# Optimization experiments

Hardware: AMD Instinct MI355X
Metric: run time of the kernel (lower is better)

Reference implementation:

```python
import jax, jax.numpy as jnp
from jax import lax
import numpy as np

ARG_NAMES = ('x w1 b1 bn1_g bn1_b bn1_m bn1_v w2 b2 bn2_g bn2_b bn2_m bn2_v w3 b3 w4 b4 '
             'attn_w attn_b attn_u g0_w1 g0_b1 g0_w2 g0_b2 g1_w1 g1_b1 g1_w2 g1_b2 '
             'g2_w1 g2_b1 g2_w2 g2_b2 c_w1 c_b1 c_w2 c_b2 c_w3 c_b3 c_w4 c_b4').split()


def _conv1d(x, w, b, stride, pad):
    # x: [N, C, L], w: [O, I, K]
    y = lax.conv_general_dilated(x, w, (stride,), [(pad, pad)],
                                 dimension_numbers=('NCH', 'OIH', 'NCH'))
    return y + b[None, :, None]


def _bn(x, g, b, m, v, eps=1e-5):
    # eval-mode BatchNorm1d over channel dim of [N, C, L]
    inv = g / jnp.sqrt(v + eps)
    return (x - m[None, :, None]) * inv[None, :, None] + b[None, :, None]


def _forward(x, w1, b1, bn1_g, bn1_b, bn1_m, bn1_v, w2, b2, bn2_g, bn2_b, bn2_m, bn2_v,
             w3, b3, w4, b4, attn_w, attn_b, attn_u,
             g0_w1, g0_b1, g0_w2, g0_b2, g1_w1, g1_b1, g1_w2, g1_b2,
             g2_w1, g2_b1, g2_w2, g2_b2,
             c_w1, c_b1, c_w2, c_b2, c_w3, c_b3, c_w4, c_b4):
    B, S, C, T = x.shape  # [batch, crops, channels=64, time=400]
    h = x.reshape(-1, C, T)
    # CNN stack (dropout = identity in eval)
    h = _bn(jax.nn.elu(_conv1d(h, w1, b1, 2, 1)), bn1_g, bn1_b, bn1_m, bn1_v)   # [N,64,192]
    h = _bn(jax.nn.elu(_conv1d(h, w2, b2, 2, 0)), bn2_g, bn2_b, bn2_m, bn2_v)   # [N,64,87]
    h = jax.nn.elu(_conv1d(h, w3, b3, 1, 0))                                    # [N,64,82]
    h = lax.reduce_window(h, 0.0, lax.add, (1, 1, 3), (1, 1, 2), 'VALID') / 3.0  # [N,64,40]
    h = jax.nn.elu(_conv1d(h, w4, b4, 1, 0))                                    # [N,64,35]
    h = h.reshape(B, S, C, -1)  # [B, S, 64, 35]
    # Attention pooling over the crop dim (dim=1), sum=True
    v = jnp.tanh(jnp.einsum('bsch,hd->bscd', h, attn_w) + attn_b)
    alphas = jax.nn.softmax(jnp.einsum('bscd,d->bsc', v, attn_u), axis=1)
    h = jax.nn.elu((h * alphas[..., None]).sum(axis=1))  # [B, 64, 35]
    # GIN over complete 64-node graph (self-loops included, eps=0):
    # aggregation per node == sum over all nodes of the graph
    def gin(h, W1, B1, W2, B2):
        agg = h + h.sum(axis=1, keepdims=True)
        return jax.nn.relu(agg @ W1 + B1) @ W2 + B2
    h = jax.nn.relu(gin(h, g0_w1, g0_b1, g0_w2, g0_b2))
    h = jax.nn.relu(gin(h, g1_w1, g1_b1, g1_w2, g1_b2))
    h = gin(h, g2_w1, g2_b1, g2_w2, g2_b2)  # no act after last layer
    # Classifier
    f = h.reshape(B, -1)  # [B, 2240]
    f = jax.nn.elu(f @ c_w1 + c_b1)
    f = jax.nn.elu(f @ c_w2 + c_b2)
    f = jax.nn.elu(f @ c_w3 + c_b3)
    return f @ c_w4 + c_b4  # [B, 2]


def setup_inputs() -> dict:
    key = jax.random.key(0)
    ks = iter(jax.random.split(key, 64))
    def rn(shape, s=0.05):
        return jax.random.normal(next(ks), shape, dtype=jnp.float32) * s
    d = {}
    d['x'] = jax.random.normal(next(ks), (32, 16, 64, 400), dtype=jnp.float32)
    d['w1'] = rn((64, 64, 20)); d['b1'] = rn((64,))
    d['bn1_g'] = jnp.ones((64,), jnp.float32); d['bn1_b'] = jnp.zeros((64,), jnp.float32)
    d['bn1_m'] = jnp.zeros((64,), jnp.float32); d['bn1_v'] = jnp.ones((64,), jnp.float32)
    d['w2'] = rn((64, 64, 20)); d['b2'] = rn((64,))
    d['bn2_g'] = jnp.ones((64,), jnp.float32); d['bn2_b'] = jnp.zeros((64,), jnp.float32)
    d['bn2_m'] = jnp.zeros((64,), jnp.float32); d['bn2_v'] = jnp.ones((64,), jnp.float32)
    d['w3'] = rn((64, 64, 6)); d['b3'] = rn((64,))
    d['w4'] = rn((64, 64, 6)); d['b4'] = rn((64,))
    d['attn_w'] = rn((35, 256), 0.1); d['attn_b'] = rn((256,), 0.1); d['attn_u'] = rn((256,), 0.1)
    d['g0_w1'] = rn((35, 256)); d['g0_b1'] = rn((256,))
    d['g0_w2'] = rn((256, 256)); d['g0_b2'] = rn((256,))
    d['g1_w1'] = rn((256, 256)); d['g1_b1'] = rn((256,))
    d['g1_w2'] = rn((256, 256)); d['g1_b2'] = rn((256,))
    d['g2_w1'] = rn((256, 35)); d['g2_b1'] = rn((35,))
    d['g2_w2'] = rn((35, 35)); d['g2_b2'] = rn((35,))
    d['c_w1'] = rn((2240, 256)); d['c_b1'] = rn((256,))
    d['c_w2'] = rn((256, 64)); d['c_b2'] = rn((64,))
    d['c_w3'] = rn((64, 16)); d['c_b3'] = rn((16,))
    d['c_w4'] = rn((16, 2)); d['c_b4'] = rn((2,))
    return d


def reference(x, w1, b1, bn1_g, bn1_b, bn1_m, bn1_v, w2, b2, bn2_g, bn2_b, bn2_m, bn2_v,
              w3, b3, w4, b4, attn_w, attn_b, attn_u,
              g0_w1, g0_b1, g0_w2, g0_b2, g1_w1, g1_b1, g1_w2, g1_b2,
              g2_w1, g2_b1, g2_w2, g2_b2,
              c_w1, c_b1, c_w2, c_b2, c_w3, c_b3, c_w4, c_b4):
    return _forward(x, w1, b1, bn1_g, bn1_b, bn1_m, bn1_v, w2, b2, bn2_g, bn2_b, bn2_m, bn2_v,
                    w3, b3, w4, b4, attn_w, attn_b, attn_u,
                    g0_w1, g0_b1, g0_w2, g0_b2, g1_w1, g1_b1, g1_w2, g1_b2,
                    g2_w1, g2_b1, g2_w2, g2_b2,
                    c_w1, c_b1, c_w2, c_b2, c_w3, c_b3, c_w4, c_b4)
```

## Files before the change

kernel.cpp:

```cpp
#include <hip/hip_runtime.h>
#include <math.h>

typedef __attribute__((ext_vector_type(8))) __bf16 bf16x8;
typedef __attribute__((ext_vector_type(4))) __bf16 bf16x4;
typedef __attribute__((ext_vector_type(4))) float f32x4;

__device__ __forceinline__ float elu_f(float v) {
    return v > 0.f ? v : (expf(v) - 1.f);
}

__global__ __launch_bounds__(256) void prep_weights(
    const float* __restrict__ w1, const float* __restrict__ w2,
    const float* __restrict__ w3, const float* __restrict__ w4,
    __bf16* __restrict__ t1, __bf16* __restrict__ t2,
    __bf16* __restrict__ t3, __bf16* __restrict__ t4)
{
    int idx = blockIdx.x * 256 + threadIdx.x;
    if (idx < 81920) {
        int k = idx / 4096, r = idx - k * 4096, co = r >> 6, ci = r & 63;
        t1[idx] = (__bf16)w1[(co * 64 + ci) * 20 + k];
    } else if (idx < 163840) {
        int j = idx - 81920;
        int k = j / 4096, r = j - k * 4096, co = r >> 6, ci = r & 63;
        t2[j] = (__bf16)w2[(co * 64 + ci) * 20 + k];
    } else if (idx < 188416) {
        int j = idx - 163840;
        int k = j / 4096, r = j - k * 4096, co = r >> 6, ci = r & 63;
        t3[j] = (__bf16)w3[(co * 64 + ci) * 6 + k];
    } else if (idx < 212992) {
        int j = idx - 188416;
        int k = j / 4096, r = j - k * 4096, co = r >> 6, ci = r & 63;
        t4[j] = (__bf16)w4[(co * 64 + ci) * 6 + k];
    }
}

__global__ __launch_bounds__(256) void prep_tr(
    const float* __restrict__ g0w1, const float* __restrict__ g0w2,
    const float* __restrict__ g1w1, const float* __restrict__ g1w2,
    const float* __restrict__ g2w1, const float* __restrict__ g2w2,
    __bf16* __restrict__ d0, __bf16* __restrict__ d1, __bf16* __restrict__ d2,
    __bf16* __restrict__ d3, __bf16* __restrict__ d4, __bf16* __restrict__ d5)
{
    int bid = blockIdx.x;
    const float* src; __bf16* dst; int K, O, Kpad, Opad, tile;
    if (bid < 4)       { src = g0w1; dst = d0; K = 35;   O = 256; Kpad = 64;   Opad = 256; tile = bid; }
    else if (bid < 20) { src = g0w2; dst = d1; K = 256;  O = 256; Kpad = 256;  Opad = 256; tile = bid - 4; }
    else if (bid < 36) { src = g1w1; dst = d2; K = 256;  O = 256; Kpad = 256;  Opad = 256; tile = bid - 20; }
    else if (bid < 52) { src = g1w2; dst = d3; K = 256;  O = 256; Kpad = 256;  Opad = 256; tile = bid - 36; }
    else if (bid < 56) { src = g2w1; dst = d4; K = 256;  O = 35;  Kpad = 256;  Opad = 64;  tile = bid - 52; }
    else               { src = g2w2; dst = d5; K = 35;   O = 35;  Kpad = 64;   Opad = 64;  tile = 0; }
    int ktiles = Kpad >> 6;
    int ot = tile / ktiles, kt = tile - ot * ktiles;
    int k0 = kt * 64, o0 = ot * 64;
    size_t LOFF = (size_t)Opad * Kpad;
    __shared__ float tl[64][68];
    int c = threadIdx.x & 63, rr = threadIdx.x >> 6;
    #pragma unroll
    for (int it = 0; it < 16; ++it) {
        int r = rr + it * 4;
        int kk = k0 + r, oo = o0 + c;
        tl[r][c] = (kk < K && oo < O) ? src[(size_t)kk * O + oo] : 0.f;
    }
    __syncthreads();
    #pragma unroll
    for (int it = 0; it < 16; ++it) {
        int r = rr + it * 4;
        float v = tl[c][r];
        __bf16 hi = (__bf16)v;
        float lo = v - (float)hi;
        size_t pos = (size_t)(o0 + r) * Kpad + k0 + c;
        dst[pos] = hi;
        dst[LOFF + pos] = (__bf16)lo;
    }
}

__global__ __launch_bounds__(512, 2) void conv1_mfma(
    const float* __restrict__ x, const __bf16* __restrict__ wT,
    const float* __restrict__ bias,
    const float* __restrict__ bn_g, const float* __restrict__ bn_b,
    const float* __restrict__ bn_m, const float* __restrict__ bn_v,
    __bf16* __restrict__ y)
{
    constexpr int LIN = 400, LOUT = 192, PAD = 1;
    constexpr int ROWS = 201;
    __shared__ __align__(16) __bf16 sx[2 * ROWS * 72];
    __shared__ __align__(16) __bf16 sw[2 * 64 * 72];

    const int tid = threadIdx.x;
    const int n = blockIdx.x;
    const int wave = tid >> 6, lane = tid & 63;
    const int m = lane & 15, quad = lane >> 4;
    const int tile = wave >> 1;
    const int coh  = (wave & 1) * 32;

    {
        const float* xg = x + (size_t)n * 64 * LIN;
        if (tid < 128) {
            int v = (tid >> 6) ? 401 : 0;
            sx[((v & 1) * ROWS + (v >> 1)) * 72 + (tid & 63)] = (__bf16)0.f;
        }
        constexpr int ITEMS = 16 * (LIN / 4);
        #pragma unroll
        for (int it = 0; it < 4; ++it) {
            int idx = it * 512 + tid;
            if (idx < ITEMS) {
                int jj = idx & 3;
                int g  = (idx >> 2) & 15;
                int q  = (idx >> 6) * 4 + jj;
                const float* xp = xg + (size_t)(4 * g) * LIN + 4 * q;
                float fa[4][4];
                #pragma unroll
                for (int u = 0; u < 4; ++u)
                    *(float4*)&fa[u][0] = *(const float4*)(xp + (size_t)u * LIN);
                #pragma unroll
                for (int e = 0; e < 4; ++e) {
                    int v = 4 * q + e + PAD;
                    bf16x4 wv = { (__bf16)fa[0][e], (__bf16)fa[1][e],
                                  (__bf16)fa[2][e], (__bf16)fa[3][e] };
                    *(bf16x4*)&sx[((v & 1) * ROWS + (v >> 1)) * 72 + 4 * g] = wv;
                }
            }
        }
    }

    f32x4 acc[3][2];
    #pragma unroll
    for (int mi = 0; mi < 3; ++mi)
        #pragma unroll
        for (int nj = 0; nj < 2; ++nj)
            acc[mi][nj] = (f32x4){0.f, 0.f, 0.f, 0.f};

    for (int kb = 0; kb < 20; kb += 2) {
        if (kb) __syncthreads();
        #pragma unroll
        for (int i = 0; i < 2; ++i) {
            int idx = i * 512 + tid;
            int r = idx >> 3, p = idx & 7;
            *(uint4*)(sw + (size_t)r * 72 + p * 8) =
                *(const uint4*)(wT + (size_t)(kb + (r >> 6)) * 4096 + (r & 63) * 64 + p * 8);
        }
        __syncthreads();

        #pragma unroll
        for (int kp2 = 0; kp2 < 2; ++kp2) {
            const int kp = kb + kp2;
            const int buf = kp & 1, rowoff = kp >> 1;
            const __bf16* abase = sx + ((size_t)buf * ROWS + tile * 48 + m + rowoff) * 72;
            const __bf16* bbase = sw + (size_t)(kp2 * 64 + coh + m) * 72;
            #pragma unroll
            for (int s = 0; s < 2; ++s) {
                bf16x8 af[3], bfr[2];
                #pragma unroll
                for (int mi = 0; mi < 3; ++mi)
                    af[mi] = *(const bf16x8*)(abase + mi * (16 * 72) + s * 32 + quad * 8);
                #pragma unroll
                for (int nj = 0; nj < 2; ++nj)
                    bfr[nj] = *(const bf16x8*)(bbase + nj * (16 * 72) + s * 32 + quad * 8);
                #pragma unroll
                for (int mi = 0; mi < 3; ++mi)
                    #pragma unroll
                    for (int nj = 0; nj < 2; ++nj)
                        acc[mi][nj] = __builtin_amdgcn_mfma_f32_16x16x32_bf16(
                            af[mi], bfr[nj], acc[mi][nj], 0, 0, 0);
            }
        }
    }

    #pragma unroll
    for (int nj = 0; nj < 2; ++nj) {
        const int co = coh + nj * 16 + m;
        const float bi = bias[co];
        const float inv   = bn_g[co] / sqrtf(bn_v[co] + 1e-5f);
        const float shift = bn_b[co] - bn_m[co] * inv;
        #pragma unroll
        for (int mi = 0; mi < 3; ++mi)
            #pragma unroll
            for (int r = 0; r < 4; ++r) {
                int t = tile * 48 + mi * 16 + quad * 4 + r;
                float v = elu_f(acc[mi][nj][r] + bi) * inv + shift;
                y[((size_t)n * LOUT + t) * 64 + co] = (__bf16)v;
            }
    }
}

__global__ __launch_bounds__(512, 2) void conv234_fused(
    const __bf16* __restrict__ h1,
    const __bf16* __restrict__ wT2, const float* __restrict__ b2,
    const float* __restrict__ bn2g, const float* __restrict__ bn2b,
    const float* __restrict__ bn2m, const float* __restrict__ bn2v,
    const __bf16* __restrict__ wT3, const float* __restrict__ b3,
    const __bf16* __restrict__ wT4, const float* __restrict__ b4,
    __bf16* __restrict__ h4)
{
    __shared__ __align__(16) __bf16 bufA[2 * 96 * 72];
    __shared__ __align__(16) __bf16 bufB[87 * 72];

    const int tid = threadIdx.x;
    const int n = blockIdx.x;
    const int wave = tid >> 6, lane = tid & 63;
    const int m = lane & 15, quad = lane >> 4;
    const int th  = wave >> 2;
    const int coq = wave & 3;

    {
        const __bf16* src = h1 + (size_t)n * 192 * 64;
        #pragma unroll
        for (int it = 0; it < 3; ++it) {
            int idx = it * 512 + tid;
            int v = idx >> 3, c8 = (idx & 7) * 8;
            *(uint4*)(bufA + ((size_t)(v & 1) * 96 + (v >> 1)) * 72 + c8) =
                *(const uint4*)(src + (size_t)v * 64 + c8);
        }
    }
    __syncthreads();

    {
        const __bf16* wb = wT2 + (size_t)(coq * 16 + m) * 64 + quad * 8;
        bf16x8 bw[20][2];
        #pragma unroll
        for (int kp = 0; kp < 20; ++kp)
            #pragma unroll
            for (int s = 0; s < 2; ++s)
                bw[kp][s] = *(const bf16x8*)(wb + (size_t)kp * 4096 + s * 32);

        f32x4 acc[3];
        #pragma unroll
        for (int mi = 0; mi < 3; ++mi) acc[mi] = (f32x4){0.f, 0.f, 0.f, 0.f};

        #pragma unroll
        for (int kp = 0; kp < 20; ++kp) {
            const int buf = kp & 1, rowoff = kp >> 1;
            const int r0 = th * 48 + m + rowoff;
            #pragma unroll
            for (int s = 0; s < 2; ++s) {
                bf16x8 af[3];
                #pragma unroll
                for (int mi = 0; mi < 3; ++mi) {
                    int rr = r0 + mi * 16; if (rr > 95) rr = 95;
                    af[mi] = *(const bf16x8*)(bufA + ((size_t)buf * 96 + rr) * 72 + s * 32 + quad * 8);
                }
                #pragma unroll
                for (int mi = 0; mi < 3; ++mi)
                    acc[mi] = __builtin_amdgcn_mfma_f32_16x16x32_bf16(
                        af[mi], bw[kp][s], acc[mi], 0, 0, 0);
            }
        }

        const int co = coq * 16 + m;
        const float bi = b2[co];
        float inv = bn2g[co] / sqrtf(bn2v[co] + 1e-5f);
        float shift = bn2b[co] - bn2m[co] * inv;
        #pragma unroll
        for (int mi = 0; mi < 3; ++mi)
            #pragma unroll
            for (int r = 0; r < 4; ++r) {
                int t = th * 48 + mi * 16 + quad * 4 + r;
                if (t < 87) {
                    float v = elu_f(acc[mi][r] + bi) * inv + shift;
                    bufB[t * 72 + co] = (__bf16)v;
                }
            }
    }
    __syncthreads();

    {
        const __bf16* wb = wT3 + (size_t)(coq * 16 + m) * 64 + quad * 8;
        bf16x8 bw[6][2];
        #pragma unroll
        for (int kp = 0; kp < 6; ++kp)
            #pragma unroll
            for (int s = 0; s < 2; ++s)
                bw[kp][s] = *(const bf16x8*)(wb + (size_t)kp * 4096 + s * 32);

        f32x4 acc[3];
        #pragma unroll
        for (int mi = 0; mi < 3; ++mi) acc[mi] = (f32x4){0.f, 0.f, 0.f, 0.f};

        #pragma unroll
        for (int kp = 0; kp < 6; ++kp) {
            const int r0 = th * 48 + m + kp;
            #pragma unroll
            for (int s = 0; s < 2; ++s) {
                bf16x8 af[3];
                #pragma unroll
                for (int mi = 0; mi < 3; ++mi) {
                    int rr = r0 + mi * 16; if (rr > 86) rr = 86;
                    af[mi] = *(const bf16x8*)(bufB + (size_t)rr * 72 + s * 32 + quad * 8);
                }
                #pragma unroll
                for (int mi = 0; mi < 3; ++mi)
                    acc[mi] = __builtin_amdgcn_mfma_f32_16x16x32_bf16(
                        af[mi], bw[kp][s], acc[mi], 0, 0, 0);
            }
        }

        const int co = coq * 16 + m;
        const float bi = b3[co];
        #pragma unroll
        for (int mi = 0; mi < 3; ++mi)
            #pragma unroll
            for (int r = 0; r < 4; ++r) {
                int t = th * 48 + mi * 16 + quad * 4 + r;
                if (t < 82)
                    bufA[t * 72 + co] = (__bf16)elu_f(acc[mi][r] + bi);
            }
    }
    __syncthreads();

    #pragma unroll
    for (int it = 0; it < 5; ++it) {
        int idx = it * 512 + tid;
        int t = idx >> 6, co = idx & 63;
        float v = ((float)bufA[(2 * t) * 72 + co] + (float)bufA[(2 * t + 1) * 72 + co] +
                   (float)bufA[(2 * t + 2) * 72 + co]) * (1.f / 3.f);
        bufB[t * 72 + co] = (__bf16)v;
    }
    __syncthreads();

    if (wave < 4) {
        const int co0 = wave * 16;
        const __bf16* wb = wT4 + (size_t)(co0 + m) * 64 + quad * 8;
        bf16x8 bw[6][2];
        #pragma unroll
        for (int kp = 0; kp < 6; ++kp)
            #pragma unroll
            for (int s = 0; s < 2; ++s)
                bw[kp][s] = *(const bf16x8*)(wb + (size_t)kp * 4096 + s * 32);

        f32x4 acc4[3];
        #pragma unroll
        for (int mi = 0; mi < 3; ++mi) acc4[mi] = (f32x4){0.f, 0.f, 0.f, 0.f};

        #pragma unroll
        for (int kp = 0; kp < 6; ++kp) {
            const int r0 = m + kp;
            #pragma unroll
            for (int s = 0; s < 2; ++s) {
                bf16x8 af[3];
                #pragma unroll
                for (int mi = 0; mi < 3; ++mi) {
                    int rr = r0 + mi * 16; if (rr > 39) rr = 39;
                    af[mi] = *(const bf16x8*)(bufB + (size_t)rr * 72 + s * 32 + quad * 8);
                }
                #pragma unroll
                for (int mi = 0; mi < 3; ++mi)
                    acc4[mi] = __builtin_amdgcn_mfma_f32_16x16x32_bf16(
                        af[mi], bw[kp][s], acc4[mi], 0, 0, 0);
            }
        }

        const int co = co0 + m;
        const float bi = b4[co];
        #pragma unroll
        for (int mi = 0; mi < 3; ++mi)
            #pragma unroll
            for (int r = 0; r < 4; ++r) {
                int t = mi * 16 + quad * 4 + r;
                if (t < 35)
                    h4[((size_t)n * 35 + t) * 64 + co] = (__bf16)elu_f(acc4[mi][r] + bi);
            }
    }
}

__global__ __launch_bounds__(256) void attn_pool_k(
    const __bf16* __restrict__ h, const float* __restrict__ W,
    const float* __restrict__ ab, const float* __restrict__ u,
    float* __restrict__ out)
{
    __shared__ float sW[35 * 256];
    __shared__ float sh[4][16 * 35 + 5];
    const int tid = threadIdx.x;
    const int pair0 = blockIdx.x * 4;
    for (int i = tid; i < 35 * 256; i += 256) sW[i] = W[i];
    for (int i = tid; i < 4 * 560; i += 256) {
        int q = i / 560, r = i - q * 560;
        int s = r / 35, t = r - s * 35;
        int bc = pair0 + q, b = bc >> 6, c = bc & 63;
        sh[q][s * 35 + t] = (float)h[(((size_t)b * 16 + s) * 35 + t) * 64 + c];
    }
    __syncthreads();

    const int wave = tid >> 6, lane = tid & 63;
    const int bc = pair0 + wave;
    const float* shw = sh[wave];

    float myu[4], myb[4];
    #pragma unroll
    for (int p = 0; p < 4; ++p) { myu[p] = u[lane + 64 * p]; myb[p] = ab[lane + 64 * p]; }

    float dot[16][4];
    #pragma unroll
    for (int s = 0; s < 16; ++s)
        #pragma unroll
        for (int p = 0; p < 4; ++p) dot[s][p] = myb[p];

    for (int t = 0; t < 35; ++t) {
        float w0 = sW[t * 256 + lane];
        float w1 = sW[t * 256 + lane + 64];
        float w2 = sW[t * 256 + lane + 128];
        float w3 = sW[t * 256 + lane + 192];
        #pragma unroll
        for (int s = 0; s < 16; ++s) {
            float hv = shw[s * 35 + t];
            dot[s][0] = fmaf(hv, w0, dot[s][0]);
            dot[s][1] = fmaf(hv, w1, dot[s][1]);
            dot[s][2] = fmaf(hv, w2, dot[s][2]);
            dot[s][3] = fmaf(hv, w3, dot[s][3]);
        }
    }

    float sc[16];
    #pragma unroll
    for (int s = 0; s < 16; ++s) {
        float v = tanhf(dot[s][0]) * myu[0] + tanhf(dot[s][1]) * myu[1]
                + tanhf(dot[s][2]) * myu[2] + tanhf(dot[s][3]) * myu[3];
        #pragma unroll
        for (int off = 1; off < 64; off <<= 1) v += __shfl_xor(v, off, 64);
        sc[s] = v;
    }

    float mx = sc[0];
    #pragma unroll
    for (int s = 1; s < 16; ++s) mx = fmaxf(mx, sc[s]);
    float e[16], sum = 0.f;
    #pragma unroll
    for (int s = 0; s < 16; ++s) { e[s] = expf(sc[s] - mx); sum += e[s]; }
    float inv = 1.f / sum;

    if (lane < 35) {
        float acc = 0.f;
        #pragma unroll
        for (int s = 0; s < 16; ++s) acc = fmaf(shw[s * 35 + lane], e[s] * inv, acc);
        out[(size_t)bc * 35 + lane] = elu_f(acc);
    }
}

#define APLANE (64 * 264)

__device__ __forceinline__ void gin_gemm_dev(
    const __bf16* As,
    const __bf16* __restrict__ Wg, int Kpad, int wlo, int Kout,
    const float* __restrict__ bias,
    int mode, __bf16* Ad, float* __restrict__ outg)
{
    const int lane = threadIdx.x & 63;
    const int wave = threadIdx.x >> 6;
    const int o0 = wave * 32;
    if (o0 >= ((Kout + 63) & ~63)) return;
    const int m = lane & 15, quad = lane >> 4;

    f32x4 acc[4][2];
    #pragma unroll
    for (int mi = 0; mi < 4; ++mi)
        #pragma unroll
        for (int nj = 0; nj < 2; ++nj)
            acc[mi][nj] = (f32x4){0.f, 0.f, 0.f, 0.f};

    for (int k0 = 0; k0 < Kpad; k0 += 32) {
        bf16x8 ah[4], al[4], bh[2], bl[2];
        #pragma unroll
        for (int mi = 0; mi < 4; ++mi) {
            const __bf16* ap = As + (size_t)(mi * 16 + m) * 264 + k0 + quad * 8;
            ah[mi] = *(const bf16x8*)ap;
            al[mi] = *(const bf16x8*)(ap + APLANE);
        }
        #pragma unroll
        for (int nj = 0; nj < 2; ++nj) {
            const __bf16* wp = Wg + (size_t)(o0 + nj * 16 + m) * Kpad + k0 + quad * 8;
            bh[nj] = *(const bf16x8*)wp;
            bl[nj] = *(const bf16x8*)(wp + wlo);
        }
        #pragma unroll
        for (int mi = 0; mi < 4; ++mi)
            #pragma unroll
            for (int nj = 0; nj < 2; ++nj) {
                acc[mi][nj] = __builtin_amdgcn_mfma_f32_16x16x32_bf16(
                    al[mi], bh[nj], acc[mi][nj], 0, 0, 0);
                acc[mi][nj] = __builtin_amdgcn_mfma_f32_16x16x32_bf16(
                    ah[mi], bl[nj], acc[mi][nj], 0, 0, 0);
                acc[mi][nj] = __builtin_amdgcn_mfma_f32_16x16x32_bf16(
                    ah[mi], bh[nj], acc[mi][nj], 0, 0, 0);
            }
    }

    #pragma unroll
    for (int nj = 0; nj < 2; ++nj) {
        const int o = o0 + nj * 16 + m;
        const bool ovalid = (o < Kout);
        const float bi = ovalid ? bias[o] : 0.f;
        float v[4][4];
        #pragma unroll
        for (int mi = 0; mi < 4; ++mi)
            #pragma unroll
            for (int r = 0; r < 4; ++r)
                v[mi][r] = acc[mi][nj][r] + bi;
        if (mode == 2) {
            if (ovalid) {
                #pragma unroll
                for (int mi = 0; mi < 4; ++mi)
                    #pragma unroll
                    for (int r = 0; r < 4; ++r)
                        outg[(size_t)(mi * 16 + quad * 4 + r) * Kout + o] = v[mi][r];
            }
        } else {
            float s = 0.f;
            #pragma unroll
            for (int mi = 0; mi < 4; ++mi)
                #pragma unroll
                for (int r = 0; r < 4; ++r) {
                    float rv = ovalid ? fmaxf(v[mi][r], 0.f) : 0.f;
                    v[mi][r] = rv;
                    s += rv;
                }
            if (mode == 1) {
                s += __shfl_xor(s, 16, 64);
                s += __shfl_xor(s, 32, 64);
            } else {
                s = 0.f;
            }
            #pragma unroll
            for (int mi = 0; mi < 4; ++mi)
                #pragma unroll
                for (int r = 0; r < 4; ++r) {
                    float a = v[mi][r] + s;
                    __bf16 hi = (__bf16)a;
                    size_t pos = (size_t)(mi * 16 + quad * 4 + r) * 264 + o;
                    Ad[pos] = hi;
                    Ad[APLANE + pos] = (__bf16)(a - (float)hi);
                }
        }
    }
}

__global__ __launch_bounds__(512) void gin_fused(
    const float* __restrict__ ha,
    const __bf16* __restrict__ gW0a, const __bf16* __restrict__ gW0b,
    const __bf16* __restrict__ gW1a, const __bf16* __restrict__ gW1b,
    const __bf16* __restrict__ gW2a, const __bf16* __restrict__ gW2b,
    const float* __restrict__ b0a, const float* __restrict__ b0b,
    const float* __restrict__ b1a, const float* __restrict__ b1b,
    const float* __restrict__ b2a, const float* __restrict__ b2b,
    float* __restrict__ H3)
{
    const int b = blockIdx.x, tid = threadIdx.x;
    __shared__ __align__(16) __bf16 sA[2][2 * APLANE];
    __shared__ float sS[64];
    const float* hab = ha + (size_t)b * 2240;

    if (tid < 64) {
        float s = 0.f;
        if (tid < 35)
            for (int n = 0; n < 64; ++n) s += hab[n * 35 + tid];
        sS[tid] = s;
    }
    __syncthreads();
    for (int idx = tid; idx < 64 * 64; idx += 512) {
        int n = idx >> 6, k = idx & 63;
        float a = (k < 35) ? hab[n * 35 + k] + sS[k] : 0.f;
        __bf16 hi = (__bf16)a;
        sA[0][n * 264 + k] = hi;
        sA[0][APLANE + n * 264 + k] = (__bf16)(a - (float)hi);
    }
    __syncthreads();

    gin_gemm_dev(sA[0], gW0a, 64,  16384, 256, b0a, 0, sA[1], nullptr); __syncthreads();
    gin_gemm_dev(sA[1], gW0b, 256, 65536, 256, b0b, 1, sA[0], nullptr); __syncthreads();
    gin_gemm_dev(sA[0], gW1a, 256, 65536, 256, b1a, 0, sA[1], nullptr); __syncthreads();
    gin_gemm_dev(sA[1], gW1b, 256, 65536, 256, b1b, 1, sA[0], nullptr); __syncthreads();
    gin_gemm_dev(sA[0], gW2a, 256, 16384, 35,  b2a, 0, sA[1], nullptr); __syncthreads();
    gin_gemm_dev(sA[1], gW2b, 64,  4096,  35,  b2b, 2, nullptr, H3 + (size_t)b * 2240);
}

__global__ __launch_bounds__(256) void cls1_part_k(
    const float* __restrict__ H3, const float* __restrict__ w1,
    float* __restrict__ s1p)
{
    const int b  = blockIdx.x;
    const int kc = blockIdx.y;
    const int k0 = kc * 140;
    __shared__ float sH[140];
    const int tid = threadIdx.x;
    if (tid < 140) sH[tid] = H3[(size_t)b * 2240 + k0 + tid];
    __syncthreads();
    const int o = (tid >> 6) * 64 + (tid & 63);
    float a0 = 0.f, a1 = 0.f, a2 = 0.f, a3 = 0.f;
    const float* wr = w1 + (size_t)k0 * 256 + o;
    #pragma unroll
    for (int k = 0; k < 140; k += 4) {
        a0 = fmaf(sH[k],     wr[(size_t)k * 256],       a0);
        a1 = fmaf(sH[k + 1], wr[(size_t)(k + 1) * 256], a1);
        a2 = fmaf(sH[k + 2], wr[(size_t)(k + 2) * 256], a2);
        a3 = fmaf(sH[k + 3], wr[(size_t)(k + 3) * 256], a3);
    }
    s1p[((size_t)kc * 32 + b) * 256 + o] = a0 + a1 + a2 + a3;
}

__global__ __launch_bounds__(256) void cls234_k(
    const float* __restrict__ s1p, const float* __restrict__ b1,
    const float* __restrict__ w2, const float* __restrict__ b2,
    const float* __restrict__ w3, const float* __restrict__ b3,
    const float* __restrict__ w4, const float* __restrict__ b4,
    float* __restrict__ out)
{
    const int b = blockIdx.x, tid = threadIdx.x;
    __shared__ float s1[256];
    __shared__ float part[4][64];
    __shared__ float s2[64];
    __shared__ float s3[16];
    {
        float acc = b1[tid];
        #pragma unroll
        for (int kc = 0; kc < 16; ++kc)
            acc += s1p[((size_t)kc * 32 + b) * 256 + tid];
        s1[tid] = elu_f(acc);
    }
    __syncthreads();
    {
        int kg = tid >> 6, o = tid & 63;
        float acc = 0.f;
        for (int k = kg * 64; k < kg * 64 + 64; ++k)
            acc = fmaf(s1[k], w2[k * 64 + o], acc);
        part[kg][o] = acc;
    }
    __syncthreads();
    if (tid < 64) {
        float acc = part[0][tid] + part[1][tid] + part[2][tid] + part[3][tid] + b2[tid];
        s2[tid] = elu_f(acc);
    }
    __syncthreads();
    if (tid < 16) {
        float acc = b3[tid];
        for (int k = 0; k < 64; ++k) acc = fmaf(s2[k], w3[k * 16 + tid], acc);
        s3[tid] = elu_f(acc);
    }
    __syncthreads();
    if (tid < 2) {
        float acc = b4[tid];
        for (int k = 0; k < 16; ++k) acc = fmaf(s3[k], w4[k * 2 + tid], acc);
        out[b * 2 + tid] = acc;
    }
}

extern "C" void kernel_launch(void* const* d_in, const int* in_sizes, int n_in,
                              void* d_out, int out_size, void* d_ws, size_t ws_size,
                              hipStream_t stream)
{
    const float* x     = (const float*)d_in[0];
    const float* w1    = (const float*)d_in[1];
    const float* b1    = (const float*)d_in[2];
    const float* bn1_g = (const float*)d_in[3];
    const float* bn1_b = (const float*)d_in[4];
    const float* bn1_m = (const float*)d_in[5];
    const float* bn1_v = (const float*)d_in[6];
    const float* w2    = (const float*)d_in[7];
    const float* b2    = (const float*)d_in[8];
    const float* bn2_g = (const float*)d_in[9];
    const float* bn2_b = (const float*)d_in[10];
    const float* bn2_m = (const float*)d_in[11];
    const float* bn2_v = (const float*)d_in[12];
    const float* w3    = (const float*)d_in[13];
    const float* b3    = (const float*)d_in[14];
    const float* w4    = (const float*)d_in[15];
    const float* b4    = (const float*)d_in[16];
    const float* attn_w = (const float*)d_in[17];
    const float* attn_b = (const float*)d_in[18];
    const float* attn_u = (const float*)d_in[19];
    const float* g0_w1 = (const float*)d_in[20];
    const float* g0_b1 = (const float*)d_in[21];
    const float* g0_w2 = (const float*)d_in[22];
    const float* g0_b2 = (const float*)d_in[23];
    const float* g1_w1 = (const float*)d_in[24];
    const float* g1_b1 = (const float*)d_in[25];
    const float* g1_w2 = (const float*)d_in[26];
    const float* g1_b2 = (const float*)d_in[27];
    const float* g2_w1 = (const float*)d_in[28];
    const float* g2_b1 = (const float*)d_in[29];
    const float* g2_w2 = (const float*)d_in[30];
    const float* g2_b2 = (const float*)d_in[31];
    const float* c_w1  = (const float*)d_in[32];
    const float* c_b1  = (const float*)d_in[33];
    const float* c_w2  = (const float*)d_in[34];
    const float* c_b2  = (const float*)d_in[35];
    const float* c_w3  = (const float*)d_in[36];
    const float* c_b3  = (const float*)d_in[37];
    const float* c_w4  = (const float*)d_in[38];
    const float* c_b4  = (const float*)d_in[39];
    float* out = (float*)d_out;

    char* ws = (char*)d_ws;
    __bf16* wT1  = (__bf16*)(ws + 0);
    __bf16* wT2  = (__bf16*)(ws + 163840);
    __bf16* wT3  = (__bf16*)(ws + 327680);
    __bf16* wT4  = (__bf16*)(ws + 376832);
    __bf16* h1   = (__bf16*)(ws + 425984);
    __bf16* h4   = (__bf16*)(ws + 13008896);
    float*  ha   = (float*)(ws + 15302656);
    __bf16* gW0a = (__bf16*)(ws + 15589376);
    __bf16* gW0b = (__bf16*)(ws + 15654912);
    __bf16* gW1a = (__bf16*)(ws + 15917056);
    __bf16* gW1b = (__bf16*)(ws + 16179200);
    __bf16* gW2a = (__bf16*)(ws + 16441344);
    __bf16* gW2b = (__bf16*)(ws + 16506880);
    float*  H3   = (float*)(ws + 16523264);
    float*  s1p  = (float*)(ws + 16809984);

    prep_weights<<<dim3(832), dim3(256), 0, stream>>>(w1, w2, w3, w4, wT1, wT2, wT3, wT4);
    prep_tr<<<dim3(57), dim3(256), 0, stream>>>(g0_w1, g0_w2, g1_w1, g1_w2, g2_w1, g2_w2,
                                                gW0a, gW0b, gW1a, gW1b, gW2a, gW2b);

    conv1_mfma<<<dim3(512), dim3(512), 0, stream>>>(
        x, wT1, b1, bn1_g, bn1_b, bn1_m, bn1_v, h1);

    conv234_fused<<<dim3(512), dim3(512), 0, stream>>>(
        h1, wT2, b2, bn2_g, bn2_b, bn2_m, bn2_v, wT3, b3, wT4, b4, h4);

    attn_pool_k<<<dim3(512), dim3(256), 0, stream>>>(h4, attn_w, attn_b, attn_u, ha);

    gin_fused<<<dim3(32), dim3(512), 0, stream>>>(
        ha, gW0a, gW0b, gW1a, gW1b, gW2a, gW2b,
        g0_b1, g0_b2, g1_b1, g1_b2, g2_b1, g2_b2, H3);

    cls1_part_k<<<dim3(32, 16), dim3(256), 0, stream>>>(H3, c_w1, s1p);
    cls234_k<<<dim3(32), dim3(256), 0, stream>>>(s1p, c_b1, c_w2, c_b2, c_w3, c_b3,
                                                 c_w4, c_b4, out);
}
```

Baseline: 298.6 us.

## Fuse conv1 into conv2-4 kernel and merge weight-prep launches

Merges the conv1 kernel into the fused conv2-4 kernel so conv1's output stays in shared memory (aliased over the input staging buffer) instead of round-tripping h1 through global memory. Conv2 weights are now staged through shared memory in k-pairs rather than held in 40 register fragments. The two weight-prep kernels are combined into one launch. The trade-offs are extra barriers in the conv2 loop, higher shared-memory use per block, and a more register-heavy single kernel that may limit occupancy.

```diff
diff --git a/kernel.cpp b/kernel.cpp
--- a/kernel.cpp
+++ b/kernel.cpp
@@ -9,39 +9,40 @@
     return v > 0.f ? v : (expf(v) - 1.f);
 }
 
-__global__ __launch_bounds__(256) void prep_weights(
+__global__ __launch_bounds__(256) void prep_all(
     const float* __restrict__ w1, const float* __restrict__ w2,
     const float* __restrict__ w3, const float* __restrict__ w4,
     __bf16* __restrict__ t1, __bf16* __restrict__ t2,
-    __bf16* __restrict__ t3, __bf16* __restrict__ t4)
-{
-    int idx = blockIdx.x * 256 + threadIdx.x;
-    if (idx < 81920) {
-        int k = idx / 4096, r = idx - k * 4096, co = r >> 6, ci = r & 63;
-        t1[idx] = (__bf16)w1[(co * 64 + ci) * 20 + k];
-    } else if (idx < 163840) {
-        int j = idx - 81920;
-        int k = j / 4096, r = j - k * 4096, co = r >> 6, ci = r & 63;
-        t2[j] = (__bf16)w2[(co * 64 + ci) * 20 + k];
-    } else if (idx < 188416) {
-        int j = idx - 163840;
-        int k = j / 4096, r = j - k * 4096, co = r >> 6, ci = r & 63;
-        t3[j] = (__bf16)w3[(co * 64 + ci) * 6 + k];
-    } else if (idx < 212992) {
-        int j = idx - 188416;
-        int k = j / 4096, r = j - k * 4096, co = r >> 6, ci = r & 63;
-        t4[j] = (__bf16)w4[(co * 64 + ci) * 6 + k];
-    }
-}
-
-__global__ __launch_bounds__(256) void prep_tr(
+    __bf16* __restrict__ t3, __bf16* __restrict__ t4,
     const float* __restrict__ g0w1, const float* __restrict__ g0w2,
     const float* __restrict__ g1w1, const float* __restrict__ g1w2,
     const float* __restrict__ g2w1, const float* __restrict__ g2w2,
     __bf16* __restrict__ d0, __bf16* __restrict__ d1, __bf16* __restrict__ d2,
     __bf16* __restrict__ d3, __bf16* __restrict__ d4, __bf16* __restrict__ d5)
 {
-    int bid = blockIdx.x;
+    __shared__ float tl[64][68];
+    const int bigbid = blockIdx.x;
+    if (bigbid < 832) {
+        int idx = bigbid * 256 + threadIdx.x;
+        if (idx < 81920) {
+            int k = idx / 4096, r = idx - k * 4096, co = r >> 6, ci = r & 63;
+            t1[idx] = (__bf16)w1[(co * 64 + ci) * 20 + k];
+        } else if (idx < 163840) {
+            int j = idx - 81920;
+            int k = j / 4096, r = j - k * 4096, co = r >> 6, ci = r & 63;
+            t2[j] = (__bf16)w2[(co * 64 + ci) * 20 + k];
+        } else if (idx < 188416) {
+            int j = idx - 163840;
+            int k = j / 4096, r = j - k * 4096, co = r >> 6, ci = r & 63;
+            t3[j] = (__bf16)w3[(co * 64 + ci) * 6 + k];
+        } else if (idx < 212992) {
+            int j = idx - 188416;
+            int k = j / 4096, r = j - k * 4096, co = r >> 6, ci = r & 63;
+            t4[j] = (__bf16)w4[(co * 64 + ci) * 6 + k];
+        }
+        return;
+    }
+    int bid = bigbid - 832;
     const float* src; __bf16* dst; int K, O, Kpad, Opad, tile;
     if (bid < 4)       { src = g0w1; dst = d0; K = 35;   O = 256; Kpad = 64;   Opad = 256; tile = bid; }
     else if (bid < 20) { src = g0w2; dst = d1; K = 256;  O = 256; Kpad = 256;  Opad = 256; tile = bid - 4; }
@@ -53,7 +54,6 @@
     int ot = tile / ktiles, kt = tile - ot * ktiles;
     int k0 = kt * 64, o0 = ot * 64;
     size_t LOFF = (size_t)Opad * Kpad;
-    __shared__ float tl[64][68];
     int c = threadIdx.x & 63, rr = threadIdx.x >> 6;
     #pragma unroll
     for (int it = 0; it < 16; ++it) {
@@ -74,24 +74,31 @@
     }
 }
 
-__global__ __launch_bounds__(512, 2) void conv1_mfma(
-    const float* __restrict__ x, const __bf16* __restrict__ wT,
-    const float* __restrict__ bias,
-    const float* __restrict__ bn_g, const float* __restrict__ bn_b,
-    const float* __restrict__ bn_m, const float* __restrict__ bn_v,
-    __bf16* __restrict__ y)
+__global__ __launch_bounds__(512, 2) void conv1234_fused(
+    const float* __restrict__ x, const __bf16* __restrict__ wT1,
+    const float* __restrict__ b1,
+    const float* __restrict__ bn1g, const float* __restrict__ bn1b,
+    const float* __restrict__ bn1m, const float* __restrict__ bn1v,
+    const __bf16* __restrict__ wT2, const float* __restrict__ b2,
+    const float* __restrict__ bn2g, const float* __restrict__ bn2b,
+    const float* __restrict__ bn2m, const float* __restrict__ bn2v,
+    const __bf16* __restrict__ wT3, const float* __restrict__ b3,
+    const __bf16* __restrict__ wT4, const float* __restrict__ b4,
+    __bf16* __restrict__ h4)
 {
-    constexpr int LIN = 400, LOUT = 192, PAD = 1;
+    constexpr int LIN = 400, PAD = 1;
     constexpr int ROWS = 201;
-    __shared__ __align__(16) __bf16 sx[2 * ROWS * 72];
+    __shared__ __align__(16) __bf16 smem[2 * ROWS * 72];
     __shared__ __align__(16) __bf16 sw[2 * 64 * 72];
+
+    __bf16* sx   = smem;
+    __bf16* bufA = smem;
+    __bf16* bufB = smem + 2 * 96 * 72;
 
     const int tid = threadIdx.x;
     const int n = blockIdx.x;
     const int wave = tid >> 6, lane = tid & 63;
     const int m = lane & 15, quad = lane >> 4;
-    const int tile = wave >> 1;
-    const int coh  = (wave & 1) * 32;
 
     {
         const float* xg = x + (size_t)n * 64 * LIN;
@@ -123,126 +130,109 @@
         }
     }
 
-    f32x4 acc[3][2];
-    #pragma unroll
-    for (int mi = 0; mi < 3; ++mi)
-        #pragma unroll
-        for (int nj = 0; nj < 2; ++nj)
-            acc[mi][nj] = (f32x4){0.f, 0.f, 0.f, 0.f};
-
-    for (int kb = 0; kb < 20; kb += 2) {
-        if (kb) __syncthreads();
-        #pragma unroll
-        for (int i = 0; i < 2; ++i) {
-            int idx = i * 512 + tid;
-            int r = idx >> 3, p = idx & 7;
-            *(uint4*)(sw + (size_t)r * 72 + p * 8) =
-                *(const uint4*)(wT + (size_t)(kb + (r >> 6)) * 4096 + (r & 63) * 64 + p * 8);
-        }
-        __syncthreads();
-
-        #pragma unroll
-        for (int kp2 = 0; kp2 < 2; ++kp2) {
-            const int kp = kb + kp2;
-            const int buf = kp & 1, rowoff = kp >> 1;
-            const __bf16* abase = sx + ((size_t)buf * ROWS + tile * 48 + m + rowoff) * 72;
-            const __bf16* bbase = sw + (size_t)(kp2 * 64 + coh + m) * 72;
-            #pragma unroll
-            for (int s = 0; s < 2; ++s) {
-                bf16x8 af[3], bfr[2];
-                #pragma unroll
-                for (int mi = 0; mi < 3; ++mi)
-                    af[mi] = *(const bf16x8*)(abase + mi * (16 * 72) + s * 32 + quad * 8);
-                #pragma unroll
-                for (int nj = 0; nj < 2; ++nj)
-                    bfr[nj] = *(const bf16x8*)(bbase + nj * (16 * 72) + s * 32 + quad * 8);
-                #pragma unroll
-                for (int mi = 0; mi < 3; ++mi)
+    const int tile = wave >> 1;
+    const int coh  = (wave & 1) * 32;
+    {
+        f32x4 acc[3][2];
+        #pragma unroll
+        for (int mi = 0; mi < 3; ++mi)
+            #pragma unroll
+            for (int nj = 0; nj < 2; ++nj)
+                acc[mi][nj] = (f32x4){0.f, 0.f, 0.f, 0.f};
+
+        for (int kb = 0; kb < 20; kb += 2) {
+            if (kb) __syncthreads();
+            #pragma unroll
+            for (int i = 0; i < 2; ++i) {
+                int idx = i * 512 + tid;
+                int r = idx >> 3, p = idx & 7;
+                *(uint4*)(sw + (size_t)r * 72 + p * 8) =
+                    *(const uint4*)(wT1 + (size_t)(kb + (r >> 6)) * 4096 + (r & 63) * 64 + p * 8);
+            }
+            __syncthreads();
+
+            #pragma unroll
+            for (int kp2 = 0; kp2 < 2; ++kp2) {
+                const int kp = kb + kp2;
+                const int buf = kp & 1, rowoff = kp >> 1;
+                const __bf16* abase = sx + ((size_t)buf * ROWS + tile * 48 + m + rowoff) * 72;
+                const __bf16* bbase = sw + (size_t)(kp2 * 64 + coh + m) * 72;
+                #pragma unroll
+                for (int s = 0; s < 2; ++s) {
+                    bf16x8 af[3], bfr[2];
+                    #pragma unroll
+                    for (int mi = 0; mi < 3; ++mi)
+                        af[mi] = *(const bf16x8*)(abase + mi * (16 * 72) + s * 32 + quad * 8);
                     #pragma unroll
                     for (int nj = 0; nj < 2; ++nj)
-                        acc[mi][nj] = __builtin_amdgcn_mfma_f32_16x16x32_bf16(
-                            af[mi], bfr[nj], acc[mi][nj], 0, 0, 0);
-            }
-        }
-    }
-
-    #pragma unroll
-    for (int nj = 0; nj < 2; ++nj) {
-        const int co = coh + nj * 16 + m;
-        const float bi = bias[co];
-        const float inv   = bn_g[co] / sqrtf(bn_v[co] + 1e-5f);
-        const float shift = bn_b[co] - bn_m[co] * inv;
-        #pragma unroll
-        for (int mi = 0; mi < 3; ++mi)
-            #pragma unroll
-            for (int r = 0; r < 4; ++r) {
-                int t = tile * 48 + mi * 16 + quad * 4 + r;
-                float v = elu_f(acc[mi][nj][r] + bi) * inv + shift;
-                y[((size_t)n * LOUT + t) * 64 + co] = (__bf16)v;
-            }
-    }
-}
-
-__global__ __launch_bounds__(512, 2) void conv234_fused(
-    const __bf16* __restrict__ h1,
-    const __bf16* __restrict__ wT2, const float* __restrict__ b2,
-    const float* __restrict__ bn2g, const float* __restrict__ bn2b,
-    const float* __restrict__ bn2m, const float* __restrict__ bn2v,
-    const __bf16* __restrict__ wT3, const float* __restrict__ b3,
-    const __bf16* __restrict__ wT4, const float* __restrict__ b4,
-    __bf16* __restrict__ h4)
-{
-    __shared__ __align__(16) __bf16 bufA[2 * 96 * 72];
-    __shared__ __align__(16) __bf16 bufB[87 * 72];
-
-    const int tid = threadIdx.x;
-    const int n = blockIdx.x;
-    const int wave = tid >> 6, lane = tid & 63;
-    const int m = lane & 15, quad = lane >> 4;
+                        bfr[nj] = *(const bf16x8*)(bbase + nj * (16 * 72) + s * 32 + quad * 8);
+                    #pragma unroll
+                    for (int mi = 0; mi < 3; ++mi)
+                        #pragma unroll
+                        for (int nj = 0; nj < 2; ++nj)
+                            acc[mi][nj] = __builtin_amdgcn_mfma_f32_16x16x32_bf16(
+                                af[mi], bfr[nj], acc[mi][nj], 0, 0, 0);
+                }
+            }
+        }
+        __syncthreads();
+
+        #pragma unroll
+        for (int nj = 0; nj < 2; ++nj) {
+            const int co = coh + nj * 16 + m;
+            const float bi = b1[co];
+            const float inv   = bn1g[co] / sqrtf(bn1v[co] + 1e-5f);
+            const float shift = bn1b[co] - bn1m[co] * inv;
+            #pragma unroll
+            for (int mi = 0; mi < 3; ++mi)
+                #pragma unroll
+                for (int r = 0; r < 4; ++r) {
+                    int t = tile * 48 + mi * 16 + quad * 4 + r;
+                    float v = elu_f(acc[mi][nj][r] + bi) * inv + shift;
+                    bufA[((size_t)(t & 1) * 96 + (t >> 1)) * 72 + co] = (__bf16)v;
+                }
+        }
+    }
+    __syncthreads();
+
     const int th  = wave >> 2;
     const int coq = wave & 3;
-
     {
-        const __bf16* src = h1 + (size_t)n * 192 * 64;
-        #pragma unroll
-        for (int it = 0; it < 3; ++it) {
-            int idx = it * 512 + tid;
-            int v = idx >> 3, c8 = (idx & 7) * 8;
-            *(uint4*)(bufA + ((size_t)(v & 1) * 96 + (v >> 1)) * 72 + c8) =
-                *(const uint4*)(src + (size_t)v * 64 + c8);
-        }
-    }
-    __syncthreads();
-
-    {
-        const __bf16* wb = wT2 + (size_t)(coq * 16 + m) * 64 + quad * 8;
-        bf16x8 bw[20][2];
-        #pragma unroll
-        for (int kp = 0; kp < 20; ++kp)
-            #pragma unroll
-            for (int s = 0; s < 2; ++s)
-                bw[kp][s] = *(const bf16x8*)(wb + (size_t)kp * 4096 + s * 32);
-
         f32x4 acc[3];
         #pragma unroll
         for (int mi = 0; mi < 3; ++mi) acc[mi] = (f32x4){0.f, 0.f, 0.f, 0.f};
 
-        #pragma unroll
-        for (int kp = 0; kp < 20; ++kp) {
-            const int buf = kp & 1, rowoff = kp >> 1;
-            const int r0 = th * 48 + m + rowoff;
-            #pragma unroll
-            for (int s = 0; s < 2; ++s) {
-                bf16x8 af[3];
-                #pragma unroll
-                for (int mi = 0; mi < 3; ++mi) {
-                    int rr = r0 + mi * 16; if (rr > 95) rr = 95;
-                    af[mi] = *(const bf16x8*)(bufA + ((size_t)buf * 96 + rr) * 72 + s * 32 + quad * 8);
-                }
-                #pragma unroll
-                for (int mi = 0; mi < 3; ++mi)
-                    acc[mi] = __builtin_amdgcn_mfma_f32_16x16x32_bf16(
-                        af[mi], bw[kp][s], acc[mi], 0, 0, 0);
+        for (int kb = 0; kb < 20; kb += 2) {
+            __syncthreads();
+            #pragma unroll
+            for (int i = 0; i < 2; ++i) {
+                int idx = i * 512 + tid;
+                int r = idx >> 3, p = idx & 7;
+                *(uint4*)(sw + (size_t)r * 72 + p * 8) =
+                    *(const uint4*)(wT2 + (size_t)(kb + (r >> 6)) * 4096 + (r & 63) * 64 + p * 8);
+            }
+            __syncthreads();
+
+            #pragma unroll
+            for (int kp2 = 0; kp2 < 2; ++kp2) {
+                const int kp = kb + kp2;
+                const int buf = kp & 1, rowoff = kp >> 1;
+                const int r0 = th * 48 + m + rowoff;
+                const __bf16* bbase = sw + (size_t)(kp2 * 64 + coq * 16 + m) * 72;
+                #pragma unroll
+                for (int s = 0; s < 2; ++s) {
+                    bf16x8 af[3], bfr;
+                    #pragma unroll
+                    for (int mi = 0; mi < 3; ++mi) {
+                        int rr = r0 + mi * 16; if (rr > 95) rr = 95;
+                        af[mi] = *(const bf16x8*)(bufA + ((size_t)buf * 96 + rr) * 72 + s * 32 + quad * 8);
+                    }
+                    bfr = *(const bf16x8*)(bbase + s * 32 + quad * 8);
+                    #pragma unroll
+                    for (int mi = 0; mi < 3; ++mi)
+                        acc[mi] = __builtin_amdgcn_mfma_f32_16x16x32_bf16(
+                            af[mi], bfr, acc[mi], 0, 0, 0);
+                }
             }
         }
 
@@ -302,7 +292,7 @@
             for (int r = 0; r < 4; ++r) {
                 int t = th * 48 + mi * 16 + quad * 4 + r;
                 if (t < 82)
-                    bufA[t * 72 + co] = (__bf16)elu_f(acc[mi][r] + bi);
+                    bufA[(size_t)t * 72 + co] = (__bf16)elu_f(acc[mi][r] + bi);
             }
     }
     __syncthreads();
@@ -692,7 +682,6 @@
     __bf16* wT2  = (__bf16*)(ws + 163840);
     __bf16* wT3  = (__bf16*)(ws + 327680);
     __bf16* wT4  = (__bf16*)(ws + 376832);
-    __bf16* h1   = (__bf16*)(ws + 425984);
     __bf16* h4   = (__bf16*)(ws + 13008896);
     float*  ha   = (float*)(ws + 15302656);
     __bf16* gW0a = (__bf16*)(ws + 15589376);
@@ -704,15 +693,15 @@
     float*  H3   = (float*)(ws + 16523264);
     float*  s1p  = (float*)(ws + 16809984);
 
-    prep_weights<<<dim3(832), dim3(256), 0, stream>>>(w1, w2, w3, w4, wT1, wT2, wT3, wT4);
-    prep_tr<<<dim3(57), dim3(256), 0, stream>>>(g0_w1, g0_w2, g1_w1, g1_w2, g2_w1, g2_w2,
-                                                gW0a, gW0b, gW1a, gW1b, gW2a, gW2b);
-
-    conv1_mfma<<<dim3(512), dim3(512), 0, stream>>>(
-        x, wT1, b1, bn1_g, bn1_b, bn1_m, bn1_v, h1);
-
-    conv234_fused<<<dim3(512), dim3(512), 0, stream>>>(
-        h1, wT2, b2, bn2_g, bn2_b, bn2_m, bn2_v, wT3, b3, wT4, b4, h4);
+    prep_all<<<dim3(889), dim3(256), 0, stream>>>(
+        w1, w2, w3, w4, wT1, wT2, wT3, wT4,
+        g0_w1, g0_w2, g1_w1, g1_w2, g2_w1, g2_w2,
+        gW0a, gW0b, gW1a, gW1b, gW2a, gW2b);
+
+    conv1234_fused<<<dim3(512), dim3(512), 0, stream>>>(
+        x, wT1, b1, bn1_g, bn1_b, bn1_m, bn1_v,
+        wT2, b2, bn2_g, bn2_b, bn2_m, bn2_v,
+        wT3, b3, wT4, b4, h4);
 
     attn_pool_k<<<dim3(512), dim3(256), 0, stream>>>(h4, attn_w, attn_b, attn_u, ha);
 
```

Measured after the change: 282.4 us. 1.06x faster.
